# Optimization experiments

Hardware: AMD Instinct MI355X
Metric: run time of the kernel (lower is better)

The kernel has to match this reference:

```python
import jax, jax.numpy as jnp
import numpy as np

B, N, C, M = 2, 16384, 256, 16  # M = win_w*win_h for stage 1
W = N // M

def setup_inputs() -> dict:
    key = jax.random.key(0)
    ks = jax.random.split(key, 8)
    s = 1.0 / np.sqrt(C)
    return {
        "input": jax.random.normal(ks[0], (B, N, C), jnp.float32),
        "embed_qk": jax.random.normal(ks[1], (B, W, M, M, 3), jnp.float32),
        "Wq": jax.random.normal(ks[2], (C, C), jnp.float32) * s,
        "bq": jax.random.normal(ks[3], (C,), jnp.float32) * 0.01,
        "Wk": jax.random.normal(ks[4], (C, C), jnp.float32) * s,
        "bk": jax.random.normal(ks[5], (C,), jnp.float32) * 0.01,
        "Wp": jax.random.normal(ks[6], (3, 1), jnp.float32) * 0.5,
        "bp": jax.random.normal(ks[7], (1,), jnp.float32) * 0.01,
    }

def reference(input, embed_qk, Wq, bq, Wk, bk, Wp, bp):
    WIN = 16  # stage==1 -> win_w*win_h = 4*4
    b, n, c = input.shape
    add = (-n) % WIN
    q = jax.nn.elu(input @ Wq + bq) + 1.0
    k = jax.nn.elu(input @ Wk + bk) + 1.0
    v = input
    pad = ((0, 0), (0, add), (0, 0))
    q_win = jnp.pad(q, pad).reshape(b, -1, WIN, c)
    k_win = jnp.pad(k, pad).reshape(b, -1, WIN, c)
    v_win = jnp.pad(v, pad).reshape(b, -1, WIN, c)
    # second ELU+1 feature map (as in the original)
    phi_q = jax.nn.elu(q_win) + 1.0
    phi_k = jax.nn.elu(k_win) + 1.0
    # KV sums over ALL windows w -> (b, m, c, d)
    KV = jnp.einsum('bwmc,bwmd->bmcd', phi_k, v_win)
    # (b, w, n, m, d) expanded intermediate
    att = jnp.einsum('bwnc,bmcd->bwnmd', phi_q, KV)
    p = (embed_qk @ Wp + bp)[..., 0]  # (b, w, m, m)
    att = att + p[..., None]
    out = att.reshape(b, -1, c)[:, :n, :]
    return out
```

## Files before the change

kernel.cpp:

```cpp
#include <hip/hip_runtime.h>

typedef __attribute__((ext_vector_type(8))) short s16x8;
typedef __attribute__((ext_vector_type(8))) ushort u16x8;
typedef __attribute__((ext_vector_type(4))) ushort u16x4;
typedef __attribute__((ext_vector_type(4))) float f32x4v;

namespace {

constexpr int kB = 2;
constexpr int kN = 16384;
constexpr int kC = 256;

__device__ __forceinline__ ushort f2bf(float f) {
  union { float f; uint u; } v; v.f = f;
  uint u = v.u + 0x7fffu + ((v.u >> 16) & 1u);
  return (ushort)(u >> 16);
}

__device__ __forceinline__ float phi_act(float x) {
  return x > 0.f ? x + 2.f : __expf(x) + 1.f;
}

template <int FM, int FN>
__device__ __forceinline__ void wave_mma(const ushort* __restrict__ A,
                                         const ushort* __restrict__ B, int ar0,
                                         int bc0, int lane,
                                         f32x4v acc[FM][FN]) {
  const int lo = lane & 15, hi = lane >> 4;
  s16x8 a[FM], b[FN];
#pragma unroll
  for (int i = 0; i < FM; ++i) {
    int r = ar0 + i * 16 + lo;
    a[i] = *reinterpret_cast<const s16x8*>(A + r * 32 + ((hi ^ ((r >> 1) & 3)) << 3));
  }
#pragma unroll
  for (int j = 0; j < FN; ++j) {
    int c = bc0 + j * 16 + lo;
    b[j] = *reinterpret_cast<const s16x8*>(B + c * 32 + ((hi ^ ((c >> 1) & 3)) << 3));
  }
#pragma unroll
  for (int i = 0; i < FM; ++i)
#pragma unroll
    for (int j = 0; j < FN; ++j)
      acc[i][j] = __builtin_amdgcn_mfma_f32_16x16x32_bf16(a[i], b[j], acc[i][j], 0, 0, 0);
}

__global__ __launch_bounds__(256) void wt_kernel(const float* __restrict__ Wq,
                                                 const float* __restrict__ Wk,
                                                 ushort* __restrict__ WqT,
                                                 ushort* __restrict__ WkT) {
  __shared__ float ts[64][65];
  const float* W = blockIdx.z ? Wk : Wq;
  ushort* WT = blockIdx.z ? WkT : WqT;
  const int bi = blockIdx.x, bj = blockIdx.y, t = threadIdx.x;
  for (int rep = 0; rep < 16; ++rep) {
    int e = rep * 256 + t, r = e >> 6, c = e & 63;
    ts[r][c] = W[(size_t)(bi * 64 + r) * kC + bj * 64 + c];
  }
  __syncthreads();
  for (int rep = 0; rep < 16; ++rep) {
    int e = rep * 256 + t, j = e >> 6, k = e & 63;
    WT[(size_t)(bj * 64 + j) * kC + bi * 64 + k] = f2bf(ts[k][j]);
  }
}

__global__ __launch_bounds__(256) void regroup_kernel(const float* __restrict__ X,
                                                      ushort* __restrict__ G) {
  __shared__ ushort ls[64 * 288];
  const int cb = blockIdx.x;
  const int wb = blockIdx.y;
  const int b = blockIdx.z;
  const int t = threadIdx.x;
  const float* src = X + ((size_t)b * kN + wb * 1024) * kC + cb * 16;
  const int lr = t >> 2, cg = t & 3;
  for (int rep = 0; rep < 16; ++rep) {
    int row = rep * 64 + lr;
    float4 v = *reinterpret_cast<const float4*>(src + (size_t)row * kC + cg * 4);
    int w = row >> 4, m = row & 15;
    int base = w * 288 + m * 18 + cg * 4;
    uint p0 = (uint)f2bf(v.x) | ((uint)f2bf(v.y) << 16);
    uint p1 = (uint)f2bf(v.z) | ((uint)f2bf(v.w) << 16);
    *reinterpret_cast<uint*>(ls + base) = p0;
    *reinterpret_cast<uint*>(ls + base + 2) = p1;
  }
  __syncthreads();
  const int m = t >> 4, c_l = t & 15;
  const size_t gbase = ((size_t)b * 16 + m) * 128 + wb * 8;
#pragma unroll
  for (int r = 0; r < 8; ++r) {
    u16x8 v;
#pragma unroll
    for (int wl = 0; wl < 8; ++wl) v[wl] = ls[(r * 8 + wl) * 288 + m * 18 + c_l];
    *reinterpret_cast<u16x8*>(G + (gbase + r) * 2048 + (size_t)(cb * 16 + c_l) * 8) = v;
  }
}

template <bool GROUPED, int RPB>
__global__ __launch_bounds__(256) void proj_kernel(const float* __restrict__ X,
                                                   const ushort* __restrict__ WT,
                                                   const float* __restrict__ bias,
                                                   ushort* __restrict__ Outp) {
  __shared__ __align__(16) ushort smem[16384];
  ushort* Alds = smem;
  ushort* Blds = smem + 4096;
  const int t = threadIdx.x, lane = t & 63, wv = t >> 6;
  const int gr0 = blockIdx.x * 128, jb = blockIdx.y, j0 = jb * 128;
  const int b = gr0 / RPB, n0 = gr0 % RPB;
  const float* Asrc = X + ((size_t)b * kN + n0) * kC;
  const ushort* Bsrc = WT + (size_t)j0 * kC;
  const int ar = t >> 2, aj = t & 3;

  float4 a0[2], a1[2];
  u16x8 rb[2];
  auto loadT = [&](int k0) {
    a0[0] = *reinterpret_cast<const float4*>(Asrc + (size_t)ar * kC + k0 + aj * 8);
    a1[0] = *reinterpret_cast<const float4*>(Asrc + (size_t)ar * kC + k0 + aj * 8 + 4);
    a0[1] = *reinterpret_cast<const float4*>(Asrc + (size_t)(ar + 64) * kC + k0 + aj * 8);
    a1[1] = *reinterpret_cast<const float4*>(Asrc + (size_t)(ar + 64) * kC + k0 + aj * 8 + 4);
    rb[0] = *reinterpret_cast<const u16x8*>(Bsrc + (size_t)ar * kC + k0 + aj * 8);
    rb[1] = *reinterpret_cast<const u16x8*>(Bsrc + (size_t)(ar + 64) * kC + k0 + aj * 8);
  };
  auto writeT = [&]() {
#pragma unroll
    for (int k = 0; k < 2; ++k) {
      int row = ar + 64 * k;
      int ch = aj ^ ((row >> 1) & 3);
      u16x8 v;
      v[0] = f2bf(a0[k].x); v[1] = f2bf(a0[k].y); v[2] = f2bf(a0[k].z); v[3] = f2bf(a0[k].w);
      v[4] = f2bf(a1[k].x); v[5] = f2bf(a1[k].y); v[6] = f2bf(a1[k].z); v[7] = f2bf(a1[k].w);
      *reinterpret_cast<u16x8*>(Alds + row * 32 + ch * 8) = v;
      *reinterpret_cast<u16x8*>(Blds + row * 32 + ch * 8) = rb[k];
    }
  };

  f32x4v acc[4][4] = {};
  const int wr0 = (wv >> 1) * 64, wc0 = (wv & 1) * 64;
  loadT(0);
  for (int ks = 0; ks < 8; ++ks) {
    __syncthreads();
    writeT();
    if (ks < 7) loadT((ks + 1) * 32);
    __syncthreads();
    wave_mma<4, 4>(Alds, Blds, wr0, wc0, lane, acc);
  }

  const int lo = lane & 15, hi = lane >> 4;
  float bv[4];
#pragma unroll
  for (int fj = 0; fj < 4; ++fj) bv[fj] = bias[j0 + wc0 + fj * 16 + lo];

  if (GROUPED) {
    __syncthreads();
#pragma unroll
    for (int fi = 0; fi < 4; ++fi)
#pragma unroll
      for (int fj = 0; fj < 4; ++fj)
#pragma unroll
        for (int r = 0; r < 4; ++r) {
          int row = wr0 + fi * 16 + hi * 4 + r;
          int col = wc0 + fj * 16 + lo;
          smem[row * 128 + col] = f2bf(phi_act(acc[fi][fj][r] + bv[fj]));
        }
    __syncthreads();
    const int wblk = n0 >> 7;
    const int mh = t >> 7, c_l = t & 127;
#pragma unroll
    for (int rep = 0; rep < 8; ++rep) {
      int m = mh * 8 + rep;
      u16x8 v;
#pragma unroll
      for (int wl = 0; wl < 8; ++wl) v[wl] = smem[(wl * 16 + m) * 128 + c_l];
      *reinterpret_cast<u16x8*>(Outp + ((((size_t)b * 16 + m) * 128 + wblk) * 256 + j0 + c_l) * 8) = v;
    }
  } else {
#pragma unroll
    for (int fi = 0; fi < 4; ++fi)
#pragma unroll
      for (int fj = 0; fj < 4; ++fj)
#pragma unroll
        for (int r = 0; r < 4; ++r) {
          int row = gr0 + wr0 + fi * 16 + hi * 4 + r;
          int col = j0 + wc0 + fj * 16 + lo;
          Outp[(size_t)row * kC + col] = f2bf(phi_act(acc[fi][fj][r] + bv[fj]));
        }
  }
}

__global__ __launch_bounds__(256) void kv_kernel(const ushort* __restrict__ Kg,
                                                 const ushort* __restrict__ Vg,
                                                 ushort* __restrict__ KVT) {
  __shared__ __align__(16) ushort smem[6144];
  ushort* Alds = smem;
  ushort* Blds = smem + 4096;
  const int t = threadIdx.x, lane = t & 63, wv = t >> 6;
  const int cb = blockIdx.x, db = blockIdx.y, bm = blockIdx.z;
  const ushort* Abase = Kg + (size_t)bm * 262144 + (size_t)(cb * 128) * 8;
  const ushort* Bbase = Vg + (size_t)bm * 262144 + (size_t)(db * 64) * 8;
  const int ac = t & 127, ajh = t >> 7;
  const int bd = t & 63, bj = t >> 6;

  u16x8 ra[2], rbv;
  auto loadT = [&](int s) {
    int w4 = s * 4;
    ra[0] = *reinterpret_cast<const u16x8*>(Abase + ((size_t)(w4 + ajh) * 256 + ac) * 8);
    ra[1] = *reinterpret_cast<const u16x8*>(Abase + ((size_t)(w4 + ajh + 2) * 256 + ac) * 8);
    rbv = *reinterpret_cast<const u16x8*>(Bbase + ((size_t)(w4 + bj) * 256 + bd) * 8);
  };
  auto writeT = [&]() {
    int sw = (ac >> 1) & 3;
    *reinterpret_cast<u16x8*>(Alds + ac * 32 + ((ajh ^ sw) << 3)) = ra[0];
    *reinterpret_cast<u16x8*>(Alds + ac * 32 + (((ajh + 2) ^ sw) << 3)) = ra[1];
    *reinterpret_cast<u16x8*>(Blds + bd * 32 + ((bj ^ ((bd >> 1) & 3)) << 3)) = rbv;
  };

  f32x4v acc[4][2] = {};
  const int wr0 = (wv >> 1) * 64, wc0 = (wv & 1) * 32;
  loadT(0);
  for (int s = 0; s < 32; ++s) {
    __syncthreads();
    writeT();
    if (s < 31) loadT(s + 1);
    __syncthreads();
    wave_mma<4, 2>(Alds, Blds, wr0, wc0, lane, acc);
  }
  const int lo = lane & 15, hi = lane >> 4;
#pragma unroll
  for (int fi = 0; fi < 4; ++fi)
#pragma unroll
    for (int fj = 0; fj < 2; ++fj) {
      int d = db * 64 + wc0 + fj * 16 + lo;
      int c = cb * 128 + wr0 + fi * 16 + hi * 4;
      u16x4 v = {f2bf(acc[fi][fj][0]), f2bf(acc[fi][fj][1]),
                 f2bf(acc[fi][fj][2]), f2bf(acc[fi][fj][3])};
      *reinterpret_cast<u16x4*>(KVT + ((size_t)bm * 256 + d) * 256 + c) = v;
    }
}

__global__ __launch_bounds__(256) void out_kernel(const ushort* __restrict__ Q,
                                                  const ushort* __restrict__ KVT,
                                                  const float* __restrict__ EQK,
                                                  const float* __restrict__ Wp,
                                                  const float* __restrict__ bp,
                                                  float* __restrict__ Out) {
  __shared__ __align__(16) ushort smem[8192];
  __shared__ float Ps[128];
  ushort* Alds = smem;
  ushort* Blds = smem + 4096;
  const int t = threadIdx.x, lane = t & 63, wv = t >> 6;
  const int qb = blockIdx.x, db = blockIdx.y, bm = blockIdx.z;
  const int b = bm >> 4, m = bm & 15;
  if (t < 128) {
    int qr = qb * 128 + t;
    const float* e = EQK + (((size_t)(b * 1024 + (qr >> 4)) * 16 + (qr & 15)) * 16 + m) * 3;
    Ps[t] = e[0] * Wp[0] + e[1] * Wp[1] + e[2] * Wp[2] + bp[0];
  }
  const ushort* Asrc = Q + ((size_t)b * 1024 + qb * 128) * kC;
  const ushort* Bsrc = KVT + (size_t)bm * 65536 + (size_t)db * 128 * kC;
  const int ar = t >> 2, aj = t & 3;

  u16x8 rga[2], rgb[2];
  auto loadT = [&](int k0) {
    rga[0] = *reinterpret_cast<const u16x8*>(Asrc + (size_t)ar * kC + k0 + aj * 8);
    rga[1] = *reinterpret_cast<const u16x8*>(Asrc + (size_t)(ar + 64) * kC + k0 + aj * 8);
    rgb[0] = *reinterpret_cast<const u16x8*>(Bsrc + (size_t)ar * kC + k0 + aj * 8);
    rgb[1] = *reinterpret_cast<const u16x8*>(Bsrc + (size_t)(ar + 64) * kC + k0 + aj * 8);
  };
  auto writeT = [&]() {
#pragma unroll
    for (int k = 0; k < 2; ++k) {
      int row = ar + 64 * k;
      int ch = aj ^ ((row >> 1) & 3);
      *reinterpret_cast<u16x8*>(Alds + row * 32 + ch * 8) = rga[k];
      *reinterpret_cast<u16x8*>(Blds + row * 32 + ch * 8) = rgb[k];
    }
  };

  f32x4v acc[4][4] = {};
  const int wr0 = (wv >> 1) * 64, wc0 = (wv & 1) * 64;
  loadT(0);
  for (int ks = 0; ks < 8; ++ks) {
    __syncthreads();
    writeT();
    if (ks < 7) loadT((ks + 1) * 32);
    __syncthreads();
    wave_mma<4, 4>(Alds, Blds, wr0, wc0, lane, acc);
  }
  const int lo = lane & 15, hi = lane >> 4;
#pragma unroll
  for (int fi = 0; fi < 4; ++fi)
#pragma unroll
    for (int r = 0; r < 4; ++r) {
      int rowl = wr0 + fi * 16 + hi * 4 + r;
      int qr = qb * 128 + rowl;
      float p = Ps[rowl];
      size_t orow = ((size_t)b * kN + (size_t)qr * 16 + m) * kC;
#pragma unroll
      for (int fj = 0; fj < 4; ++fj) {
        int d = db * 128 + wc0 + fj * 16 + lo;
        Out[orow + d] = acc[fi][fj][r] + p;
      }
    }
}

}

extern "C" void kernel_launch(void* const* d_in, const int* in_sizes, int n_in,
                              void* d_out, int out_size, void* d_ws,
                              size_t ws_size, hipStream_t stream) {
  const float* input = (const float*)d_in[0];
  const float* eqk = (const float*)d_in[1];
  const float* Wq = (const float*)d_in[2];
  const float* bq = (const float*)d_in[3];
  const float* Wk = (const float*)d_in[4];
  const float* bk = (const float*)d_in[5];
  const float* Wp = (const float*)d_in[6];
  const float* bp = (const float*)d_in[7];
  float* out = (float*)d_out;

  ushort* ws = (ushort*)d_ws;
  ushort* WqT = ws;
  ushort* WkT = WqT + 65536;
  ushort* xg = WkT + 65536;
  ushort* kg = xg + 8388608;
  ushort* qf = kg + 8388608;
  ushort* kvt = qf + 524288;

  wt_kernel<<<dim3(4, 4, 2), 256, 0, stream>>>(Wq, Wk, WqT, WkT);
  regroup_kernel<<<dim3(16, 16, 2), 256, 0, stream>>>(input, xg);
  proj_kernel<true, 16384><<<dim3(256, 2), 256, 0, stream>>>(input, WkT, bk, kg);
  proj_kernel<false, 1024><<<dim3(16, 2), 256, 0, stream>>>(input, WqT, bq, qf);
  kv_kernel<<<dim3(2, 4, 32), 256, 0, stream>>>(kg, xg, kvt);
  out_kernel<<<dim3(8, 2, 32), 256, 0, stream>>>(qf, kvt, eqk, Wp, bp, out);
}
```

Before: 163.8 us.

## Fuse regroup and Q/K projections into one kernel with double-buffered LDS pipelines

The separate regroup, K-projection and Q-projection kernels are merged into one 512-thread kernel. Each block computes all 256 output columns and writes the bf16 regrouped input as a side effect, so the input is read once instead of several times. The kv, out and projection kernels now use double-buffered LDS with one barrier per k-step and sched_barrier hints. The kv kernel retiles to 64x64 blocks with a deeper k-chunk, doubling its grid. The cost is higher LDS use and more registers per block, which may lower occupancy, and the fused kernel's A-tile loads are strided scalar fp32 reads.

```diff
diff --git a/kernel.cpp b/kernel.cpp
--- a/kernel.cpp
+++ b/kernel.cpp
@@ -10,6 +10,7 @@
 constexpr int kB = 2;
 constexpr int kN = 16384;
 constexpr int kC = 256;
+constexpr int kQR = 1024;
 
 __device__ __forceinline__ ushort f2bf(float f) {
   union { float f; uint u; } v; v.f = f;
@@ -19,30 +20,6 @@
 
 __device__ __forceinline__ float phi_act(float x) {
   return x > 0.f ? x + 2.f : __expf(x) + 1.f;
-}
-
-template <int FM, int FN>
-__device__ __forceinline__ void wave_mma(const ushort* __restrict__ A,
-                                         const ushort* __restrict__ B, int ar0,
-                                         int bc0, int lane,
-                                         f32x4v acc[FM][FN]) {
-  const int lo = lane & 15, hi = lane >> 4;
-  s16x8 a[FM], b[FN];
-#pragma unroll
-  for (int i = 0; i < FM; ++i) {
-    int r = ar0 + i * 16 + lo;
-    a[i] = *reinterpret_cast<const s16x8*>(A + r * 32 + ((hi ^ ((r >> 1) & 3)) << 3));
-  }
-#pragma unroll
-  for (int j = 0; j < FN; ++j) {
-    int c = bc0 + j * 16 + lo;
-    b[j] = *reinterpret_cast<const s16x8*>(B + c * 32 + ((hi ^ ((c >> 1) & 3)) << 3));
-  }
-#pragma unroll
-  for (int i = 0; i < FM; ++i)
-#pragma unroll
-    for (int j = 0; j < FN; ++j)
-      acc[i][j] = __builtin_amdgcn_mfma_f32_16x16x32_bf16(a[i], b[j], acc[i][j], 0, 0, 0);
 }
 
 __global__ __launch_bounds__(256) void wt_kernel(const float* __restrict__ Wq,
@@ -64,240 +41,315 @@
   }
 }
 
-__global__ __launch_bounds__(256) void regroup_kernel(const float* __restrict__ X,
-                                                      ushort* __restrict__ G) {
-  __shared__ ushort ls[64 * 288];
-  const int cb = blockIdx.x;
-  const int wb = blockIdx.y;
-  const int b = blockIdx.z;
-  const int t = threadIdx.x;
-  const float* src = X + ((size_t)b * kN + wb * 1024) * kC + cb * 16;
-  const int lr = t >> 2, cg = t & 3;
-  for (int rep = 0; rep < 16; ++rep) {
-    int row = rep * 64 + lr;
-    float4 v = *reinterpret_cast<const float4*>(src + (size_t)row * kC + cg * 4);
-    int w = row >> 4, m = row & 15;
-    int base = w * 288 + m * 18 + cg * 4;
-    uint p0 = (uint)f2bf(v.x) | ((uint)f2bf(v.y) << 16);
-    uint p1 = (uint)f2bf(v.z) | ((uint)f2bf(v.w) << 16);
-    *reinterpret_cast<uint*>(ls + base) = p0;
-    *reinterpret_cast<uint*>(ls + base + 2) = p1;
-  }
+__global__ __launch_bounds__(512) void proj_fused(
+    const float* __restrict__ X, const ushort* __restrict__ WqT,
+    const ushort* __restrict__ WkT, const float* __restrict__ bq,
+    const float* __restrict__ bk, ushort* __restrict__ xg,
+    ushort* __restrict__ kg, ushort* __restrict__ qf) {
+  __shared__ __align__(16) ushort smem[24576];
+
+  const int t = threadIdx.x, lane = t & 63, wv = t >> 6;
+  const int bx = blockIdx.x;
+  const bool kmode = bx < 256;
+  int b, n0;
+  const ushort* WT;
+  const float* bias;
+  if (kmode) {
+    b = bx >> 7; n0 = (bx & 127) * 128; WT = WkT; bias = bk;
+  } else {
+    int i = bx - 256; b = i >> 3; n0 = (i & 7) * 128; WT = WqT; bias = bq;
+  }
+  const int wgrp = bx & 127;
+  const float* Xbase = X + ((size_t)b * kN + n0) * kC;
+
+  const int m = t >> 5, cl = t & 31;
+  const int bj = t >> 2, bch = t & 3;
+
+  float fa[8];
+  u16x8 rb0, rb1;
+  auto stageLoad = [&](int ks) {
+    const int k0 = ks * 32;
+#pragma unroll
+    for (int wl = 0; wl < 8; ++wl)
+      fa[wl] = Xbase[(size_t)(wl * 16 + m) * kC + k0 + cl];
+    rb0 = *reinterpret_cast<const u16x8*>(WT + (size_t)bj * kC + k0 + bch * 8);
+    rb1 = *reinterpret_cast<const u16x8*>(WT + (size_t)(bj + 128) * kC + k0 + bch * 8);
+  };
+  auto stageWrite = [&](int h, int ks) {
+    ushort* A = smem + h * 4096;
+    ushort* B = smem + 8192 + h * 8192;
+    u16x8 vx;
+#pragma unroll
+    for (int wl = 0; wl < 8; ++wl) {
+      int row = wl * 16 + m;
+      ushort bf = f2bf(fa[wl]);
+      A[row * 32 + (((cl >> 3) ^ ((row >> 1) & 3)) << 3) + (cl & 7)] = bf;
+      vx[wl] = bf;
+    }
+    *reinterpret_cast<u16x8*>(B + bj * 32 + ((bch ^ ((bj >> 1) & 3)) << 3)) = rb0;
+    *reinterpret_cast<u16x8*>(B + (bj + 128) * 32 + ((bch ^ (((bj + 128) >> 1) & 3)) << 3)) = rb1;
+    if (kmode) {
+      *reinterpret_cast<u16x8*>(
+          xg + (((size_t)(b * 16 + m) * 128 + wgrp) * 256 + ks * 32 + cl) * 8) = vx;
+    }
+  };
+
+  f32x4v acc[4][4] = {};
+  const int lo = lane & 15, hi = lane >> 4;
+  const int wr0 = (wv >> 2) * 64, wc0 = (wv & 3) * 64;
+  auto mma = [&](int h) {
+    const ushort* A = smem + h * 4096;
+    const ushort* B = smem + 8192 + h * 8192;
+    s16x8 af[4], bf[4];
+#pragma unroll
+    for (int i = 0; i < 4; ++i) {
+      int r = wr0 + i * 16 + lo;
+      af[i] = *reinterpret_cast<const s16x8*>(A + r * 32 + ((hi ^ ((r >> 1) & 3)) << 3));
+    }
+#pragma unroll
+    for (int j = 0; j < 4; ++j) {
+      int cj = wc0 + j * 16 + lo;
+      bf[j] = *reinterpret_cast<const s16x8*>(B + cj * 32 + ((hi ^ ((cj >> 1) & 3)) << 3));
+    }
+#pragma unroll
+    for (int i = 0; i < 4; ++i)
+#pragma unroll
+      for (int j = 0; j < 4; ++j)
+        acc[i][j] = __builtin_amdgcn_mfma_f32_16x16x32_bf16(af[i], bf[j], acc[i][j], 0, 0, 0);
+  };
+
+  stageLoad(0);
+  stageWrite(0, 0);
   __syncthreads();
-  const int m = t >> 4, c_l = t & 15;
-  const size_t gbase = ((size_t)b * 16 + m) * 128 + wb * 8;
-#pragma unroll
-  for (int r = 0; r < 8; ++r) {
-    u16x8 v;
-#pragma unroll
-    for (int wl = 0; wl < 8; ++wl) v[wl] = ls[(r * 8 + wl) * 288 + m * 18 + c_l];
-    *reinterpret_cast<u16x8*>(G + (gbase + r) * 2048 + (size_t)(cb * 16 + c_l) * 8) = v;
-  }
-}
-
-template <bool GROUPED, int RPB>
-__global__ __launch_bounds__(256) void proj_kernel(const float* __restrict__ X,
-                                                   const ushort* __restrict__ WT,
-                                                   const float* __restrict__ bias,
-                                                   ushort* __restrict__ Outp) {
+  int cur = 0;
+  for (int ks = 0; ks < 8; ++ks) {
+    if (ks < 7) stageLoad(ks + 1);
+    __builtin_amdgcn_sched_barrier(0);
+    mma(cur);
+    __builtin_amdgcn_sched_barrier(0);
+    if (ks < 7) stageWrite(cur ^ 1, ks + 1);
+    __syncthreads();
+    cur ^= 1;
+  }
+
+  float bv[4];
+#pragma unroll
+  for (int fj = 0; fj < 4; ++fj) bv[fj] = bias[wc0 + fj * 16 + lo];
+
+  if (kmode) {
+    u16x8 vout[8];
+    ushort* ep = smem;
+#pragma unroll
+    for (int h = 0; h < 2; ++h) {
+      __syncthreads();
+      if ((wv >> 2) == h) {
+#pragma unroll
+        for (int fi = 0; fi < 4; ++fi)
+#pragma unroll
+          for (int fj = 0; fj < 4; ++fj)
+#pragma unroll
+            for (int r4 = 0; r4 < 4; ++r4) {
+              int rl = fi * 16 + hi * 4 + r4;
+              int col = wc0 + fj * 16 + lo;
+              ep[rl * 260 + col] = f2bf(phi_act(acc[fi][fj][r4] + bv[fj]));
+            }
+      }
+      __syncthreads();
+#pragma unroll
+      for (int j = 0; j < 8; ++j) {
+        int c = j * 32 + cl;
+#pragma unroll
+        for (int wl = 0; wl < 4; ++wl)
+          vout[j][h * 4 + wl] = ep[(wl * 16 + m) * 260 + c];
+      }
+    }
+#pragma unroll
+    for (int j = 0; j < 8; ++j) {
+      int c = j * 32 + cl;
+      *reinterpret_cast<u16x8*>(
+          kg + (((size_t)(b * 16 + m) * 128 + wgrp) * 256 + c) * 8) = vout[j];
+    }
+  } else {
+#pragma unroll
+    for (int fi = 0; fi < 4; ++fi)
+#pragma unroll
+      for (int fj = 0; fj < 4; ++fj)
+#pragma unroll
+        for (int r4 = 0; r4 < 4; ++r4) {
+          int row = n0 + wr0 + fi * 16 + hi * 4 + r4;
+          int col = wc0 + fj * 16 + lo;
+          qf[((size_t)b * kQR + row) * kC + col] = f2bf(phi_act(acc[fi][fj][r4] + bv[fj]));
+        }
+  }
+}
+
+__global__ __launch_bounds__(256) void kv_kernel(const ushort* __restrict__ kg,
+                                                 const ushort* __restrict__ xg,
+                                                 ushort* __restrict__ kvt) {
   __shared__ __align__(16) ushort smem[16384];
-  ushort* Alds = smem;
-  ushort* Blds = smem + 4096;
-  const int t = threadIdx.x, lane = t & 63, wv = t >> 6;
-  const int gr0 = blockIdx.x * 128, jb = blockIdx.y, j0 = jb * 128;
-  const int b = gr0 / RPB, n0 = gr0 % RPB;
-  const float* Asrc = X + ((size_t)b * kN + n0) * kC;
-  const ushort* Bsrc = WT + (size_t)j0 * kC;
-  const int ar = t >> 2, aj = t & 3;
-
-  float4 a0[2], a1[2];
-  u16x8 rb[2];
-  auto loadT = [&](int k0) {
-    a0[0] = *reinterpret_cast<const float4*>(Asrc + (size_t)ar * kC + k0 + aj * 8);
-    a1[0] = *reinterpret_cast<const float4*>(Asrc + (size_t)ar * kC + k0 + aj * 8 + 4);
-    a0[1] = *reinterpret_cast<const float4*>(Asrc + (size_t)(ar + 64) * kC + k0 + aj * 8);
-    a1[1] = *reinterpret_cast<const float4*>(Asrc + (size_t)(ar + 64) * kC + k0 + aj * 8 + 4);
-    rb[0] = *reinterpret_cast<const u16x8*>(Bsrc + (size_t)ar * kC + k0 + aj * 8);
-    rb[1] = *reinterpret_cast<const u16x8*>(Bsrc + (size_t)(ar + 64) * kC + k0 + aj * 8);
-  };
-  auto writeT = [&]() {
-#pragma unroll
-    for (int k = 0; k < 2; ++k) {
-      int row = ar + 64 * k;
-      int ch = aj ^ ((row >> 1) & 3);
-      u16x8 v;
-      v[0] = f2bf(a0[k].x); v[1] = f2bf(a0[k].y); v[2] = f2bf(a0[k].z); v[3] = f2bf(a0[k].w);
-      v[4] = f2bf(a1[k].x); v[5] = f2bf(a1[k].y); v[6] = f2bf(a1[k].z); v[7] = f2bf(a1[k].w);
-      *reinterpret_cast<u16x8*>(Alds + row * 32 + ch * 8) = v;
-      *reinterpret_cast<u16x8*>(Blds + row * 32 + ch * 8) = rb[k];
-    }
-  };
-
-  f32x4v acc[4][4] = {};
-  const int wr0 = (wv >> 1) * 64, wc0 = (wv & 1) * 64;
-  loadT(0);
-  for (int ks = 0; ks < 8; ++ks) {
-    __syncthreads();
-    writeT();
-    if (ks < 7) loadT((ks + 1) * 32);
-    __syncthreads();
-    wave_mma<4, 4>(Alds, Blds, wr0, wc0, lane, acc);
-  }
-
-  const int lo = lane & 15, hi = lane >> 4;
-  float bv[4];
-#pragma unroll
-  for (int fj = 0; fj < 4; ++fj) bv[fj] = bias[j0 + wc0 + fj * 16 + lo];
-
-  if (GROUPED) {
-    __syncthreads();
-#pragma unroll
-    for (int fi = 0; fi < 4; ++fi)
-#pragma unroll
-      for (int fj = 0; fj < 4; ++fj)
-#pragma unroll
-        for (int r = 0; r < 4; ++r) {
-          int row = wr0 + fi * 16 + hi * 4 + r;
-          int col = wc0 + fj * 16 + lo;
-          smem[row * 128 + col] = f2bf(phi_act(acc[fi][fj][r] + bv[fj]));
-        }
-    __syncthreads();
-    const int wblk = n0 >> 7;
-    const int mh = t >> 7, c_l = t & 127;
-#pragma unroll
-    for (int rep = 0; rep < 8; ++rep) {
-      int m = mh * 8 + rep;
-      u16x8 v;
-#pragma unroll
-      for (int wl = 0; wl < 8; ++wl) v[wl] = smem[(wl * 16 + m) * 128 + c_l];
-      *reinterpret_cast<u16x8*>(Outp + ((((size_t)b * 16 + m) * 128 + wblk) * 256 + j0 + c_l) * 8) = v;
-    }
-  } else {
-#pragma unroll
-    for (int fi = 0; fi < 4; ++fi)
-#pragma unroll
-      for (int fj = 0; fj < 4; ++fj)
-#pragma unroll
-        for (int r = 0; r < 4; ++r) {
-          int row = gr0 + wr0 + fi * 16 + hi * 4 + r;
-          int col = j0 + wc0 + fj * 16 + lo;
-          Outp[(size_t)row * kC + col] = f2bf(phi_act(acc[fi][fj][r] + bv[fj]));
-        }
-  }
-}
-
-__global__ __launch_bounds__(256) void kv_kernel(const ushort* __restrict__ Kg,
-                                                 const ushort* __restrict__ Vg,
-                                                 ushort* __restrict__ KVT) {
-  __shared__ __align__(16) ushort smem[6144];
-  ushort* Alds = smem;
-  ushort* Blds = smem + 4096;
   const int t = threadIdx.x, lane = t & 63, wv = t >> 6;
   const int cb = blockIdx.x, db = blockIdx.y, bm = blockIdx.z;
-  const ushort* Abase = Kg + (size_t)bm * 262144 + (size_t)(cb * 128) * 8;
-  const ushort* Bbase = Vg + (size_t)bm * 262144 + (size_t)(db * 64) * 8;
-  const int ac = t & 127, ajh = t >> 7;
-  const int bd = t & 63, bj = t >> 6;
-
-  u16x8 ra[2], rbv;
-  auto loadT = [&](int s) {
-    int w4 = s * 4;
-    ra[0] = *reinterpret_cast<const u16x8*>(Abase + ((size_t)(w4 + ajh) * 256 + ac) * 8);
-    ra[1] = *reinterpret_cast<const u16x8*>(Abase + ((size_t)(w4 + ajh + 2) * 256 + ac) * 8);
-    rbv = *reinterpret_cast<const u16x8*>(Bbase + ((size_t)(w4 + bj) * 256 + bd) * 8);
-  };
-  auto writeT = [&]() {
-    int sw = (ac >> 1) & 3;
-    *reinterpret_cast<u16x8*>(Alds + ac * 32 + ((ajh ^ sw) << 3)) = ra[0];
-    *reinterpret_cast<u16x8*>(Alds + ac * 32 + (((ajh + 2) ^ sw) << 3)) = ra[1];
-    *reinterpret_cast<u16x8*>(Blds + bd * 32 + ((bj ^ ((bd >> 1) & 3)) << 3)) = rbv;
-  };
-
-  f32x4v acc[4][2] = {};
-  const int wr0 = (wv >> 1) * 64, wc0 = (wv & 1) * 32;
-  loadT(0);
-  for (int s = 0; s < 32; ++s) {
+  const int lc = t & 63, g2 = t >> 6;
+
+  u16x8 ra0, ra1, rb0, rb1;
+  auto stageLoad = [&](int ws) {
+    size_t base = (size_t)bm * 128 + ws * 8;
+    ra0 = *reinterpret_cast<const u16x8*>(kg + ((base + g2) * 256 + cb * 64 + lc) * 8);
+    ra1 = *reinterpret_cast<const u16x8*>(kg + ((base + g2 + 4) * 256 + cb * 64 + lc) * 8);
+    rb0 = *reinterpret_cast<const u16x8*>(xg + ((base + g2) * 256 + db * 64 + lc) * 8);
+    rb1 = *reinterpret_cast<const u16x8*>(xg + ((base + g2 + 4) * 256 + db * 64 + lc) * 8);
+  };
+  auto stageWrite = [&](int h) {
+    ushort* A = smem + h * 4096;
+    ushort* B = smem + 8192 + h * 4096;
+    int s = (lc >> 1) & 7;
+    *reinterpret_cast<u16x8*>(A + lc * 64 + ((g2 ^ s) << 3)) = ra0;
+    *reinterpret_cast<u16x8*>(A + lc * 64 + (((g2 + 4) ^ s) << 3)) = ra1;
+    *reinterpret_cast<u16x8*>(B + lc * 64 + ((g2 ^ s) << 3)) = rb0;
+    *reinterpret_cast<u16x8*>(B + lc * 64 + (((g2 + 4) ^ s) << 3)) = rb1;
+  };
+
+  f32x4v acc[2][2] = {};
+  const int lo = lane & 15, hi = lane >> 4;
+  const int wr0 = (wv >> 1) * 32, wc0 = (wv & 1) * 32;
+  auto mma = [&](int h) {
+    const ushort* A = smem + h * 4096;
+    const ushort* B = smem + 8192 + h * 4096;
+    s16x8 af[2][2], bf[2][2];
+#pragma unroll
+    for (int i = 0; i < 2; ++i) {
+      int r = wr0 + i * 16 + lo;
+      int s = (r >> 1) & 7;
+#pragma unroll
+      for (int kk = 0; kk < 2; ++kk)
+        af[i][kk] = *reinterpret_cast<const s16x8*>(A + r * 64 + (((kk * 4 + hi) ^ s) << 3));
+    }
+#pragma unroll
+    for (int j = 0; j < 2; ++j) {
+      int c = wc0 + j * 16 + lo;
+      int s = (c >> 1) & 7;
+#pragma unroll
+      for (int kk = 0; kk < 2; ++kk)
+        bf[j][kk] = *reinterpret_cast<const s16x8*>(B + c * 64 + (((kk * 4 + hi) ^ s) << 3));
+    }
+#pragma unroll
+    for (int kk = 0; kk < 2; ++kk)
+#pragma unroll
+      for (int i = 0; i < 2; ++i)
+#pragma unroll
+        for (int j = 0; j < 2; ++j)
+          acc[i][j] = __builtin_amdgcn_mfma_f32_16x16x32_bf16(af[i][kk], bf[j][kk], acc[i][j], 0, 0, 0);
+  };
+
+  stageLoad(0);
+  stageWrite(0);
+  __syncthreads();
+  int cur = 0;
+  for (int ws = 0; ws < 16; ++ws) {
+    if (ws < 15) stageLoad(ws + 1);
+    __builtin_amdgcn_sched_barrier(0);
+    mma(cur);
+    __builtin_amdgcn_sched_barrier(0);
+    if (ws < 15) stageWrite(cur ^ 1);
     __syncthreads();
-    writeT();
-    if (s < 31) loadT(s + 1);
-    __syncthreads();
-    wave_mma<4, 2>(Alds, Blds, wr0, wc0, lane, acc);
-  }
-  const int lo = lane & 15, hi = lane >> 4;
-#pragma unroll
-  for (int fi = 0; fi < 4; ++fi)
-#pragma unroll
-    for (int fj = 0; fj < 2; ++fj) {
-      int d = db * 64 + wc0 + fj * 16 + lo;
-      int c = cb * 128 + wr0 + fi * 16 + hi * 4;
-      u16x4 v = {f2bf(acc[fi][fj][0]), f2bf(acc[fi][fj][1]),
-                 f2bf(acc[fi][fj][2]), f2bf(acc[fi][fj][3])};
-      *reinterpret_cast<u16x4*>(KVT + ((size_t)bm * 256 + d) * 256 + c) = v;
-    }
-}
-
-__global__ __launch_bounds__(256) void out_kernel(const ushort* __restrict__ Q,
-                                                  const ushort* __restrict__ KVT,
-                                                  const float* __restrict__ EQK,
-                                                  const float* __restrict__ Wp,
-                                                  const float* __restrict__ bp,
-                                                  float* __restrict__ Out) {
-  __shared__ __align__(16) ushort smem[8192];
+    cur ^= 1;
+  }
+#pragma unroll
+  for (int i = 0; i < 2; ++i)
+#pragma unroll
+    for (int j = 0; j < 2; ++j) {
+      int d = db * 64 + wc0 + j * 16 + lo;
+      int c = cb * 64 + wr0 + i * 16 + hi * 4;
+      u16x4 v = {f2bf(acc[i][j][0]), f2bf(acc[i][j][1]), f2bf(acc[i][j][2]),
+                 f2bf(acc[i][j][3])};
+      *reinterpret_cast<u16x4*>(kvt + ((size_t)bm * 256 + d) * 256 + c) = v;
+    }
+}
+
+__global__ __launch_bounds__(256) void out_kernel(
+    const ushort* __restrict__ qf, const ushort* __restrict__ kvt,
+    const float* __restrict__ EQK, const float* __restrict__ Wp,
+    const float* __restrict__ bp, float* __restrict__ Out) {
+  __shared__ __align__(16) ushort smem[16384];
   __shared__ float Ps[128];
-  ushort* Alds = smem;
-  ushort* Blds = smem + 4096;
   const int t = threadIdx.x, lane = t & 63, wv = t >> 6;
   const int qb = blockIdx.x, db = blockIdx.y, bm = blockIdx.z;
-  const int b = bm >> 4, m = bm & 15;
+  const int b = bm >> 4, mm = bm & 15;
   if (t < 128) {
     int qr = qb * 128 + t;
-    const float* e = EQK + (((size_t)(b * 1024 + (qr >> 4)) * 16 + (qr & 15)) * 16 + m) * 3;
+    const float* e = EQK + (((size_t)(b * 1024 + (qr >> 4)) * 16 + (qr & 15)) * 16 + mm) * 3;
     Ps[t] = e[0] * Wp[0] + e[1] * Wp[1] + e[2] * Wp[2] + bp[0];
   }
-  const ushort* Asrc = Q + ((size_t)b * 1024 + qb * 128) * kC;
-  const ushort* Bsrc = KVT + (size_t)bm * 65536 + (size_t)db * 128 * kC;
-  const int ar = t >> 2, aj = t & 3;
-
-  u16x8 rga[2], rgb[2];
-  auto loadT = [&](int k0) {
-    rga[0] = *reinterpret_cast<const u16x8*>(Asrc + (size_t)ar * kC + k0 + aj * 8);
-    rga[1] = *reinterpret_cast<const u16x8*>(Asrc + (size_t)(ar + 64) * kC + k0 + aj * 8);
-    rgb[0] = *reinterpret_cast<const u16x8*>(Bsrc + (size_t)ar * kC + k0 + aj * 8);
-    rgb[1] = *reinterpret_cast<const u16x8*>(Bsrc + (size_t)(ar + 64) * kC + k0 + aj * 8);
-  };
-  auto writeT = [&]() {
-#pragma unroll
-    for (int k = 0; k < 2; ++k) {
-      int row = ar + 64 * k;
-      int ch = aj ^ ((row >> 1) & 3);
-      *reinterpret_cast<u16x8*>(Alds + row * 32 + ch * 8) = rga[k];
-      *reinterpret_cast<u16x8*>(Blds + row * 32 + ch * 8) = rgb[k];
-    }
+  const int r2 = t >> 2, ch = t & 3;
+
+  u16x8 ra0, ra1, rb0, rb1;
+  auto stageLoad = [&](int ks) {
+    int k0 = ks * 32;
+    const ushort* Aq = qf + ((size_t)b * kQR + qb * 128) * kC;
+    const ushort* Bk = kvt + ((size_t)bm * 256 + db * 128) * kC;
+    ra0 = *reinterpret_cast<const u16x8*>(Aq + (size_t)r2 * kC + k0 + ch * 8);
+    ra1 = *reinterpret_cast<const u16x8*>(Aq + (size_t)(r2 + 64) * kC + k0 + ch * 8);
+    rb0 = *reinterpret_cast<const u16x8*>(Bk + (size_t)r2 * kC + k0 + ch * 8);
+    rb1 = *reinterpret_cast<const u16x8*>(Bk + (size_t)(r2 + 64) * kC + k0 + ch * 8);
+  };
+  auto stageWrite = [&](int h) {
+    ushort* A = smem + h * 4096;
+    ushort* B = smem + 8192 + h * 4096;
+    *reinterpret_cast<u16x8*>(A + r2 * 32 + ((ch ^ ((r2 >> 1) & 3)) << 3)) = ra0;
+    *reinterpret_cast<u16x8*>(A + (r2 + 64) * 32 + ((ch ^ (((r2 + 64) >> 1) & 3)) << 3)) = ra1;
+    *reinterpret_cast<u16x8*>(B + r2 * 32 + ((ch ^ ((r2 >> 1) & 3)) << 3)) = rb0;
+    *reinterpret_cast<u16x8*>(B + (r2 + 64) * 32 + ((ch ^ (((r2 + 64) >> 1) & 3)) << 3)) = rb1;
   };
 
   f32x4v acc[4][4] = {};
+  const int lo = lane & 15, hi = lane >> 4;
   const int wr0 = (wv >> 1) * 64, wc0 = (wv & 1) * 64;
-  loadT(0);
+  auto mma = [&](int h) {
+    const ushort* A = smem + h * 4096;
+    const ushort* B = smem + 8192 + h * 4096;
+    s16x8 af[4], bf[4];
+#pragma unroll
+    for (int i = 0; i < 4; ++i) {
+      int r = wr0 + i * 16 + lo;
+      af[i] = *reinterpret_cast<const s16x8*>(A + r * 32 + ((hi ^ ((r >> 1) & 3)) << 3));
+    }
+#pragma unroll
+    for (int j = 0; j < 4; ++j) {
+      int c = wc0 + j * 16 + lo;
+      bf[j] = *reinterpret_cast<const s16x8*>(B + c * 32 + ((hi ^ ((c >> 1) & 3)) << 3));
+    }
+#pragma unroll
+    for (int i = 0; i < 4; ++i)
+#pragma unroll
+      for (int j = 0; j < 4; ++j)
+        acc[i][j] = __builtin_amdgcn_mfma_f32_16x16x32_bf16(af[i], bf[j], acc[i][j], 0, 0, 0);
+  };
+
+  stageLoad(0);
+  stageWrite(0);
+  __syncthreads();
+  int cur = 0;
   for (int ks = 0; ks < 8; ++ks) {
+    if (ks < 7) stageLoad(ks + 1);
+    __builtin_amdgcn_sched_barrier(0);
+    mma(cur);
+    __builtin_amdgcn_sched_barrier(0);
+    if (ks < 7) stageWrite(cur ^ 1);
     __syncthreads();
-    writeT();
-    if (ks < 7) loadT((ks + 1) * 32);
-    __syncthreads();
-    wave_mma<4, 4>(Alds, Blds, wr0, wc0, lane, acc);
-  }
-  const int lo = lane & 15, hi = lane >> 4;
+    cur ^= 1;
+  }
 #pragma unroll
   for (int fi = 0; fi < 4; ++fi)
 #pragma unroll
-    for (int r = 0; r < 4; ++r) {
-      int rowl = wr0 + fi * 16 + hi * 4 + r;
+    for (int r4 = 0; r4 < 4; ++r4) {
+      int rowl = wr0 + fi * 16 + hi * 4 + r4;
       int qr = qb * 128 + rowl;
       float p = Ps[rowl];
-      size_t orow = ((size_t)b * kN + (size_t)qr * 16 + m) * kC;
+      size_t orow = ((size_t)b * kN + (size_t)qr * 16 + mm) * kC;
 #pragma unroll
       for (int fj = 0; fj < 4; ++fj) {
         int d = db * 128 + wc0 + fj * 16 + lo;
-        Out[orow + d] = acc[fi][fj][r] + p;
+        Out[orow + d] = acc[fi][fj][r4] + p;
       }
     }
 }
@@ -326,9 +378,7 @@
   ushort* kvt = qf + 524288;
 
   wt_kernel<<<dim3(4, 4, 2), 256, 0, stream>>>(Wq, Wk, WqT, WkT);
-  regroup_kernel<<<dim3(16, 16, 2), 256, 0, stream>>>(input, xg);
-  proj_kernel<true, 16384><<<dim3(256, 2), 256, 0, stream>>>(input, WkT, bk, kg);
-  proj_kernel<false, 1024><<<dim3(16, 2), 256, 0, stream>>>(input, WqT, bq, qf);
-  kv_kernel<<<dim3(2, 4, 32), 256, 0, stream>>>(kg, xg, kvt);
+  proj_fused<<<dim3(272), 512, 0, stream>>>(input, WqT, WkT, bq, bk, xg, kg, qf);
+  kv_kernel<<<dim3(4, 4, 32), 256, 0, stream>>>(kg, xg, kvt);
   out_kernel<<<dim3(8, 2, 32), 256, 0, stream>>>(qf, kvt, eqk, Wp, bp, out);
 }
```

Result: faster. 143.7 us (-12.2%).
